# Kernel optimization log

Measured on AMD Instinct MI355X. Metric: run time of the kernel, lower is better.

## Reference

```python
import jax, jax.numpy as jnp
import numpy as np

NUM_HEADS = 32


def setup_inputs() -> dict:
    key = jax.random.key(0)
    k1, k2, k3 = jax.random.split(key, 3)
    B, C = 8192, 4096
    x = jax.random.normal(k1, (B, C), dtype=jnp.float32)
    w_qkv = jax.random.normal(k2, (3 * C, C), dtype=jnp.float32) * (C ** -0.5)
    w_proj = jax.random.normal(k3, (C, C), dtype=jnp.float32) * (C ** -0.5)
    b_proj = jnp.zeros((C,), dtype=jnp.float32)
    return {"x": x, "w_qkv": w_qkv, "w_proj": w_proj, "b_proj": b_proj}


def reference(x, w_qkv, w_proj, b_proj):
    B, C = x.shape
    H = NUM_HEADS
    hd = C // H
    scale = hd ** -0.5
    # qkv projection: (B, 3C) -> (B, 3, H, hd)
    qkv = (x @ w_qkv.T).reshape(B, 3, H, hd)
    q, k, v = qkv[:, 0], qkv[:, 1], qkv[:, 2]  # each (B, H, hd)
    # tiny per-row attention over heads: scores (B, H, H)
    attn = jax.nn.softmax(jnp.einsum("bhd,bgd->bhg", q, k) * scale, axis=-1)
    out = jnp.einsum("bhg,bgd->bhd", attn, v)  # (B, H, hd)
    # faithful to torch: transpose(1,2) then reshape -> head-dim-major flatten
    out = out.transpose(0, 2, 1).reshape(B, C)
    return out @ w_proj.T + b_proj
```

## Files before the change

kernel.cpp:

```cpp
#include <hip/hip_runtime.h>
#include <hip/hip_bf16.h>
#include <stdint.h>

typedef __attribute__((ext_vector_type(8))) short bf16x8;
typedef __attribute__((ext_vector_type(4))) float f32x4;
typedef __hip_bfloat16 bf16;

typedef const __attribute__((address_space(1))) void* gas_ptr;
typedef __attribute__((address_space(3))) void* las_ptr;

__device__ __forceinline__ void async_load16(const bf16* g, bf16* l) {
  __builtin_amdgcn_global_load_lds((gas_ptr)g, (las_ptr)l, 16, 0, 0);
}

#define BAR() __builtin_amdgcn_s_barrier()
#define LGKM0() asm volatile("s_waitcnt lgkmcnt(0)")
#define LGKM8() asm volatile("s_waitcnt lgkmcnt(8)")
#define VMCNT6() asm volatile("s_waitcnt vmcnt(6)")
#define VMCNT0() asm volatile("s_waitcnt vmcnt(0)")

__global__ __launch_bounds__(256) void cvt_kernel(
    const float* __restrict__ in, bf16* __restrict__ out, int n8) {
  int i = blockIdx.x * blockDim.x + threadIdx.x;
  if (i >= n8) return;
  const float4* p = (const float4*)in;
  float4 a = p[2 * i], b = p[2 * i + 1];
  union { bf16x8 v; bf16 h[8]; } u;
  u.h[0] = __float2bfloat16(a.x); u.h[1] = __float2bfloat16(a.y);
  u.h[2] = __float2bfloat16(a.z); u.h[3] = __float2bfloat16(a.w);
  u.h[4] = __float2bfloat16(b.x); u.h[5] = __float2bfloat16(b.y);
  u.h[6] = __float2bfloat16(b.z); u.h[7] = __float2bfloat16(b.w);
  ((bf16x8*)out)[i] = u.v;
}


__device__ __forceinline__ bf16x8 ld_frag(const bf16* buf, int rl, int j) {
  return *(const bf16x8*)(buf + rl * 64 + ((j ^ (rl & 7)) << 3));
}

__device__ __forceinline__ void stage_halfA(const bf16* __restrict__ G,
                                            int row0, int K, int kt, bf16* buf,
                                            int r0, int wv, int lane) {
#pragma unroll
  for (int c = 0; c < 2; ++c) {
    const int sl = c * 512 + wv * 64 + lane;
    const int rl = r0 + (sl >> 3);
    const int j = (sl & 7) ^ (rl & 7);
    const int grow = ((rl >> 6) & 1) * 128 + ((rl >> 7) & 1) * 64 + (rl & 63);
    async_load16(G + (size_t)(row0 + grow) * K + kt + j * 8,
                 buf + r0 * 64 + c * 4096 + wv * 512);
  }
}

__device__ __forceinline__ void stage_halfB(const bf16* __restrict__ G,
                                            int row0, int K, int kt, bf16* buf,
                                            int r0, int wv, int lane) {
#pragma unroll
  for (int c = 0; c < 2; ++c) {
    const int sl = c * 512 + wv * 64 + lane;
    const int rl = r0 + (sl >> 3);
    const int j = (sl & 7) ^ (rl & 7);
    const int grow = ((rl >> 5) & 3) * 64 + ((rl >> 7) & 1) * 32 + (rl & 31);
    async_load16(G + (size_t)(row0 + grow) * K + kt + j * 8,
                 buf + r0 * 64 + c * 4096 + wv * 512);
  }
}

#define READ_A(DST, BUF, QM)                                                  \
  {                                                                           \
    _Pragma("unroll") for (int tm = 0; tm < 4; ++tm) {                        \
      _Pragma("unroll") for (int ks = 0; ks < 2; ++ks) {                      \
        DST[tm * 2 + ks] =                                                    \
            ld_frag(BUF, (QM) * 128 + wm * 64 + tm * 16 + l15, ks * 4 + quad);\
      }                                                                       \
    }                                                                         \
  }

#define READ_B(DST, BUF, QN)                                                  \
  {                                                                           \
    _Pragma("unroll") for (int tn = 0; tn < 2; ++tn) {                        \
      _Pragma("unroll") for (int ks = 0; ks < 2; ++ks) {                      \
        DST[tn * 2 + ks] =                                                    \
            ld_frag(BUF, (QN) * 128 + wn * 32 + tn * 16 + l15, ks * 4 + quad);\
      }                                                                       \
    }                                                                         \
  }

#define MFMA_Q(QM, QN, AF, BF)                                                \
  {                                                                           \
    __builtin_amdgcn_s_setprio(1);                                            \
    _Pragma("unroll") for (int tm = 0; tm < 4; ++tm) {                        \
      _Pragma("unroll") for (int tn = 0; tn < 2; ++tn) {                      \
        _Pragma("unroll") for (int ks = 0; ks < 2; ++ks) {                    \
          acc[(QM) * 4 + tm][(QN) * 2 + tn] =                                 \
              __builtin_amdgcn_mfma_f32_16x16x32_bf16(                        \
                  AF[tm * 2 + ks], BF[tn * 2 + ks],                           \
                  acc[(QM) * 4 + tm][(QN) * 2 + tn], 0, 0, 0);                \
        }                                                                     \
      }                                                                       \
    }                                                                         \
    __builtin_amdgcn_s_setprio(0);                                            \
  }

template <int BIAS, typename OutT>
__global__ __launch_bounds__(512, 2) void gemm256_kernel(
    const bf16* __restrict__ A, const bf16* __restrict__ B,
    const float* __restrict__ bias, OutT* __restrict__ C,
    int M, int N, int K) {
  __shared__ __attribute__((aligned(16))) bf16 sA[2][256 * 64];
  __shared__ __attribute__((aligned(16))) bf16 sB[2][256 * 64];

  const int tid = threadIdx.x;
  const int lane = tid & 63;
  const int wv = tid >> 6;
  const int wm = wv >> 2;
  const int wn = wv & 3;
  const int quad = lane >> 4;
  const int l15 = lane & 15;

  const int nwg = gridDim.x;
  const int bid = blockIdx.x;
  const int wg = (bid & 7) * (nwg >> 3) + (bid >> 3);
  const int nby = M >> 8;
  const int by = wg % nby;
  const int bx = wg / nby;
  const int m0 = by * 256;
  const int n0 = bx * 256;

  const int NT = K >> 6;
  const int klast = (NT - 1) << 6;

  f32x4 acc[8][4];
  const f32x4 zero = {0.f, 0.f, 0.f, 0.f};
#pragma unroll
  for (int i = 0; i < 8; ++i)
#pragma unroll
    for (int j = 0; j < 4; ++j) acc[i][j] = zero;

  stage_halfA(A, m0, K, 0, sA[0], 0, wv, lane);
  stage_halfB(B, n0, K, 0, sB[0], 0, wv, lane);
  stage_halfB(B, n0, K, 0, sB[0], 128, wv, lane);
  stage_halfA(A, m0, K, 0, sA[0], 128, wv, lane);
  stage_halfA(A, m0, K, 64, sA[1], 0, wv, lane);
  stage_halfB(B, n0, K, 64, sB[1], 0, wv, lane);
  stage_halfB(B, n0, K, 64, sB[1], 128, wv, lane);
  VMCNT6();
  BAR();

  for (int it = 0; it < (NT >> 1); ++it) {
    const int kt0 = it << 7;
    const int kt1 = kt0 + 64;
    const int ks0 = (kt0 + 128 < klast) ? kt0 + 128 : klast;
    const int ks1 = (kt0 + 192 < klast) ? kt0 + 192 : klast;

    bf16x8 a0f[8], a1f[8], b0f[4], b1f[4];

    READ_A(a0f, sA[0], 0);
    READ_B(b0f, sB[0], 0);
    stage_halfA(A, m0, K, kt1, sA[1], 128, wv, lane);
    LGKM8();
    BAR(); LGKM0();
    MFMA_Q(0, 0, a0f, b0f);
    BAR();
    READ_B(b1f, sB[0], 1);
    stage_halfA(A, m0, K, ks0, sA[0], 0, wv, lane);
    BAR(); LGKM0();
    MFMA_Q(0, 1, a0f, b1f);
    BAR();
    READ_A(a1f, sA[0], 1);
    stage_halfB(B, n0, K, ks0, sB[0], 0, wv, lane);
    BAR(); LGKM0();
    MFMA_Q(1, 0, a1f, b0f);
    BAR();
    stage_halfB(B, n0, K, ks0, sB[0], 128, wv, lane);
    BAR(); LGKM0();
    MFMA_Q(1, 1, a1f, b1f);
    VMCNT6();
    BAR();

    READ_A(a0f, sA[1], 0);
    READ_B(b0f, sB[1], 0);
    stage_halfA(A, m0, K, ks0, sA[0], 128, wv, lane);
    LGKM8();
    BAR(); LGKM0();
    MFMA_Q(0, 0, a0f, b0f);
    BAR();
    READ_B(b1f, sB[1], 1);
    stage_halfA(A, m0, K, ks1, sA[1], 0, wv, lane);
    BAR(); LGKM0();
    MFMA_Q(0, 1, a0f, b1f);
    BAR();
    READ_A(a1f, sA[1], 1);
    stage_halfB(B, n0, K, ks1, sB[1], 0, wv, lane);
    BAR(); LGKM0();
    MFMA_Q(1, 0, a1f, b0f);
    BAR();
    stage_halfB(B, n0, K, ks1, sB[1], 128, wv, lane);
    BAR(); LGKM0();
    MFMA_Q(1, 1, a1f, b1f);
    VMCNT6();
    BAR();
  }

  VMCNT0();

#pragma unroll
  for (int mf = 0; mf < 8; ++mf) {
    const int row0 = m0 + wm * 128 + (mf >> 2) * 64 + (mf & 3) * 16 + quad * 4;
#pragma unroll
    for (int nf = 0; nf < 4; ++nf) {
      const int col = n0 + wn * 64 + (nf >> 1) * 32 + (nf & 1) * 16 + l15;
      float bv = 0.f;
      if (BIAS) bv = bias[col];
#pragma unroll
      for (int i = 0; i < 4; ++i) {
        float v = acc[mf][nf][i] + bv;
        if constexpr (sizeof(OutT) == 2)
          C[(size_t)(row0 + i) * N + col] = __float2bfloat16(v);
        else
          C[(size_t)(row0 + i) * N + col] = v;
      }
    }
  }
}

__global__ __launch_bounds__(256) void attn_kernel(
    const bf16* __restrict__ qkv, bf16* __restrict__ out) {
  const int b = blockIdx.x;
  const int tid = threadIdx.x;
  __shared__ uint32_t sQKV[3 * 32 * 65];
  __shared__ float S[32][33];

  const uint32_t* src = (const uint32_t*)(qkv + (size_t)b * 12288);
#pragma unroll
  for (int i = 0; i < 24; ++i) {
    int c = tid + i * 256;
    int sec = c >> 11;
    int cc = c & 2047;
    int row = cc >> 6;
    int col = cc & 63;
    sQKV[sec * 2080 + row * 65 + col] = src[c];
  }
  __syncthreads();

  const float scale = 0.088388347648318447f;
#pragma unroll
  for (int i = 0; i < 4; ++i) {
    int p = tid + i * 256;
    int h = p >> 5;
    int g = p & 31;
    const __hip_bfloat162* qr = (const __hip_bfloat162*)(sQKV + h * 65);
    const __hip_bfloat162* kr = (const __hip_bfloat162*)(sQKV + 2080 + g * 65);
    float acc = 0.f;
#pragma unroll
    for (int d = 0; d < 64; ++d) {
      float2 qf = __bfloat1622float2(qr[d]);
      float2 kf = __bfloat1622float2(kr[d]);
      acc = fmaf(qf.x, kf.x, acc);
      acc = fmaf(qf.y, kf.y, acc);
    }
    S[h][g] = acc * scale;
  }
  __syncthreads();

  if (tid < 32) {
    float m = -1e30f;
#pragma unroll
    for (int g = 0; g < 32; ++g) m = fmaxf(m, S[tid][g]);
    float sum = 0.f;
#pragma unroll
    for (int g = 0; g < 32; ++g) {
      float e = __expf(S[tid][g] - m);
      S[tid][g] = e;
      sum += e;
    }
    float inv = 1.f / sum;
#pragma unroll
    for (int g = 0; g < 32; ++g) S[tid][g] *= inv;
  }
  __syncthreads();

  const bf16* V = (const bf16*)(sQKV + 2 * 2080);
  bf16* orow = out + (size_t)b * 4096;
#pragma unroll
  for (int i = 0; i < 16; ++i) {
    int c = tid + i * 256;
    int d = c >> 5;
    int h = c & 31;
    float acc = 0.f;
#pragma unroll
    for (int g = 0; g < 32; ++g)
      acc = fmaf(S[h][g], __bfloat162float(V[g * 130 + d]), acc);
    orow[c] = __float2bfloat16(acc);
  }
}

extern "C" void kernel_launch(void* const* d_in, const int* in_sizes, int n_in,
                              void* d_out, int out_size, void* d_ws, size_t ws_size,
                              hipStream_t stream) {
  const float* x      = (const float*)d_in[0];
  const float* w_qkv  = (const float*)d_in[1];
  const float* w_proj = (const float*)d_in[2];
  const float* b_proj = (const float*)d_in[3];
  float* out = (float*)d_out;

  const int C = in_sizes[3];
  const int B = in_sizes[0] / C;

  bf16* xb    = (bf16*)d_ws;
  bf16* wqb   = xb + (size_t)B * C;
  bf16* qkvb  = wqb + (size_t)3 * C * C;
  bf16* attnb = xb;
  bf16* wpb   = wqb;

  const int nx = B * C / 8, nwq = 3 * C * C / 8, nwp = C * C / 8;
  cvt_kernel<<<(nx + 255) / 256, 256, 0, stream>>>(x, xb, nx);
  cvt_kernel<<<(nwq + 255) / 256, 256, 0, stream>>>(w_qkv, wqb, nwq);

  gemm256_kernel<0, bf16><<<(3 * C / 256) * (B / 256), 512, 0, stream>>>(
      xb, wqb, nullptr, qkvb, B, 3 * C, C);
  attn_kernel<<<B, 256, 0, stream>>>(qkvb, attnb);
  cvt_kernel<<<(nwp + 255) / 256, 256, 0, stream>>>(w_proj, wpb, nwp);
  gemm256_kernel<1, float><<<(C / 256) * (B / 256), 512, 0, stream>>>(
      attnb, wpb, b_proj, out, B, C, C);
}
```

Before: 1.774 ms.

## Prefetch LDS fragments one phase ahead and drop explicit lgkmcnt waits in GEMM loop

Restructures the main GEMM loop so the LDS fragment reads for the next MFMA quadrant, and for the next k-tile, are issued before the current MFMAs run. Fragment registers become persistent and double-buffered. The change removes the explicit lgkmcnt waits and several barriers per phase, and shifts the vmcnt wait earlier. The goal is to overlap LDS reads with MFMA work and cut synchronisation stalls. In exchange it raises register pressure, and it relies on the compiler to insert correct LDS waits, which risks races on the staged buffers.

```diff
diff --git a/kernel.cpp b/kernel.cpp
--- a/kernel.cpp
+++ b/kernel.cpp
@@ -14,8 +14,7 @@
 }
 
 #define BAR() __builtin_amdgcn_s_barrier()
-#define LGKM0() asm volatile("s_waitcnt lgkmcnt(0)")
-#define LGKM8() asm volatile("s_waitcnt lgkmcnt(8)")
+#define VMCNT4() asm volatile("s_waitcnt vmcnt(4)")
 #define VMCNT6() asm volatile("s_waitcnt vmcnt(6)")
 #define VMCNT0() asm volatile("s_waitcnt vmcnt(0)")
 
@@ -137,6 +136,8 @@
 #pragma unroll
     for (int j = 0; j < 4; ++j) acc[i][j] = zero;
 
+  bf16x8 Ae[8], Ao[8], Be[4], Bo[4];
+
   stage_halfA(A, m0, K, 0, sA[0], 0, wv, lane);
   stage_halfB(B, n0, K, 0, sB[0], 0, wv, lane);
   stage_halfB(B, n0, K, 0, sB[0], 128, wv, lane);
@@ -146,6 +147,8 @@
   stage_halfB(B, n0, K, 64, sB[1], 128, wv, lane);
   VMCNT6();
   BAR();
+  READ_A(Ae, sA[0], 0);
+  READ_B(Be, sB[0], 0);
 
   for (int it = 0; it < (NT >> 1); ++it) {
     const int kt0 = it << 7;
@@ -153,52 +156,39 @@
     const int ks0 = (kt0 + 128 < klast) ? kt0 + 128 : klast;
     const int ks1 = (kt0 + 192 < klast) ? kt0 + 192 : klast;
 
-    bf16x8 a0f[8], a1f[8], b0f[4], b1f[4];
-
-    READ_A(a0f, sA[0], 0);
-    READ_B(b0f, sB[0], 0);
+    READ_B(Bo, sB[0], 1);
     stage_halfA(A, m0, K, kt1, sA[1], 128, wv, lane);
-    LGKM8();
-    BAR(); LGKM0();
-    MFMA_Q(0, 0, a0f, b0f);
-    BAR();
-    READ_B(b1f, sB[0], 1);
+    MFMA_Q(0, 0, Ae, Be);
+    BAR();
+    READ_A(Ao, sA[0], 1);
     stage_halfA(A, m0, K, ks0, sA[0], 0, wv, lane);
-    BAR(); LGKM0();
-    MFMA_Q(0, 1, a0f, b1f);
-    BAR();
-    READ_A(a1f, sA[0], 1);
+    MFMA_Q(0, 1, Ae, Bo);
+    BAR();
     stage_halfB(B, n0, K, ks0, sB[0], 0, wv, lane);
-    BAR(); LGKM0();
-    MFMA_Q(1, 0, a1f, b0f);
-    BAR();
+    MFMA_Q(1, 0, Ao, Be);
+    VMCNT4();
+    BAR();
+    READ_A(Ae, sA[1], 0);
+    READ_B(Be, sB[1], 0);
     stage_halfB(B, n0, K, ks0, sB[0], 128, wv, lane);
-    BAR(); LGKM0();
-    MFMA_Q(1, 1, a1f, b1f);
-    VMCNT6();
-    BAR();
-
-    READ_A(a0f, sA[1], 0);
-    READ_B(b0f, sB[1], 0);
+    MFMA_Q(1, 1, Ao, Bo);
+    BAR();
+    READ_B(Bo, sB[1], 1);
     stage_halfA(A, m0, K, ks0, sA[0], 128, wv, lane);
-    LGKM8();
-    BAR(); LGKM0();
-    MFMA_Q(0, 0, a0f, b0f);
-    BAR();
-    READ_B(b1f, sB[1], 1);
+    MFMA_Q(0, 0, Ae, Be);
+    BAR();
+    READ_A(Ao, sA[1], 1);
     stage_halfA(A, m0, K, ks1, sA[1], 0, wv, lane);
-    BAR(); LGKM0();
-    MFMA_Q(0, 1, a0f, b1f);
-    BAR();
-    READ_A(a1f, sA[1], 1);
+    MFMA_Q(0, 1, Ae, Bo);
+    BAR();
     stage_halfB(B, n0, K, ks1, sB[1], 0, wv, lane);
-    BAR(); LGKM0();
-    MFMA_Q(1, 0, a1f, b0f);
-    BAR();
+    MFMA_Q(1, 0, Ao, Be);
+    VMCNT4();
+    BAR();
+    READ_A(Ae, sA[0], 0);
+    READ_B(Be, sB[0], 0);
     stage_halfB(B, n0, K, ks1, sB[1], 128, wv, lane);
-    BAR(); LGKM0();
-    MFMA_Q(1, 1, a1f, b1f);
-    VMCNT6();
+    MFMA_Q(1, 1, Ao, Bo);
     BAR();
   }
 
```

New measurement: 1.859 ms. +4.8%, slower.
